# Optimization experiments

Hardware: AMD Instinct MI355X
Metric: run time of the kernel (lower is better)

## Reference

```python
import jax, jax.numpy as jnp
import numpy as np

NB_HEADS = 12


def setup_inputs() -> dict:
    key = jax.random.key(0)
    ks = jax.random.split(key, 6)
    B, S, D, H = 4, 1024, 768, NB_HEADS
    x = jax.random.normal(ks[0], (B, S, D), dtype=jnp.float32)
    Wqkv = jax.random.normal(ks[1], (D, 3 * D), dtype=jnp.float32) * 0.02
    bqkv = jnp.zeros((3 * D,), dtype=jnp.float32)
    Wl = jax.random.normal(ks[2], (H, H), dtype=jnp.float32) * 0.3
    bl = jnp.zeros((H,), dtype=jnp.float32)
    Ww = jax.random.normal(ks[3], (H, H), dtype=jnp.float32) * 0.3
    bw = jnp.zeros((H,), dtype=jnp.float32)
    Wproj = jax.random.normal(ks[4], (D, D), dtype=jnp.float32) * 0.02
    bproj = jnp.zeros((D,), dtype=jnp.float32)
    return {"x": x, "Wqkv": Wqkv, "bqkv": bqkv, "Wl": Wl, "bl": bl,
            "Ww": Ww, "bw": bw, "Wproj": Wproj, "bproj": bproj}


def reference(x, Wqkv, bqkv, Wl, bl, Ww, bw, Wproj, bproj):
    B, S, D = x.shape
    H = NB_HEADS
    dh = D // H
    scale = dh ** (-0.5)
    # qkv projection: [B,S,3D] -> [3,B,H,S,dh]
    qkv = (x @ Wqkv + bqkv).reshape(B, S, 3, H, dh).transpose(2, 0, 3, 1, 4)
    q, k, v = qkv[0] * scale, qkv[1], qkv[2]
    # raw attention logits [B,H,S,S]
    attn = jnp.einsum('bhqd,bhkd->bhqk', q, k)
    # pre-softmax talking-heads mix across head dim (Dense over heads)
    attn = jnp.einsum('bhqk,hg->bgqk', attn, Wl) + bl[None, :, None, None]
    attn = jax.nn.softmax(attn, axis=-1)
    # post-softmax talking-heads mix
    attn = jnp.einsum('bhqk,hg->bgqk', attn, Ww) + bw[None, :, None, None]
    # attention-weighted values -> [B,S,D]
    out = jnp.einsum('bhqk,bhkd->bqhd', attn, v).reshape(B, S, D)
    return out @ Wproj + bproj
```

## Files before the change

kernel.cpp:

```cpp
#include <hip/hip_runtime.h>
#include <cstdint>

#define BB 4
#define SS 1024
#define DD 768
#define HH 12
#define DH 64

typedef unsigned short u16;
typedef unsigned int   u32;
typedef __attribute__((ext_vector_type(8))) short bf16x8;
typedef __attribute__((ext_vector_type(4))) float f32x4;

__device__ __forceinline__ u16 f2bf(float f) {
    u32 u = __float_as_uint(f);
    u += 0x7fffu + ((u >> 16) & 1u);
    return (u16)(u >> 16);
}
__device__ __forceinline__ float b2f(u32 lo16) {
    return __uint_as_float(lo16 << 16);
}
__device__ __forceinline__ u32 pack2(float a, float b) {
    return (u32)f2bf(a) | ((u32)f2bf(b) << 16);
}

#define ASYNC16(gp, lp) __builtin_amdgcn_global_load_lds( \
    (const __attribute__((address_space(1))) void*)(gp),  \
    (__attribute__((address_space(3))) void*)(lp), 16, 0, 0)

template<int BM_, int BN_, class Epi>
__device__ __forceinline__ void mfma_gemm(
    const u16* __restrict__ A, const u16* __restrict__ B,
    int K, int lda, int ldb, int m0, int n0, const Epi& epi)
{
    constexpr int MI = BM_ / 32;
    constexpr int NJ = BN_ / 32;
    __shared__ u16 Alds[BM_ * 32];
    __shared__ u16 Blds[BN_ * 32];

    const int tid  = threadIdx.x;
    const int wave = tid >> 6;
    const int lane = tid & 63;
    const int wr = wave >> 1, wc = wave & 1;

    const int ar = lane >> 2;
    const int ac = (lane & 3) * 8;

    f32x4 acc[MI][NJ] = {};

    for (int k0 = 0; k0 < K; k0 += 32) {
        __syncthreads();
#pragma unroll
        for (int j = 0; j < BM_ / 64; ++j) {
            const int rb = wave * (BM_ / 4) + j * 16;
            ASYNC16(A + (size_t)(m0 + rb + ar) * lda + k0 + ac, &Alds[rb * 32]);
        }
#pragma unroll
        for (int j = 0; j < BN_ / 64; ++j) {
            const int rb = wave * (BN_ / 4) + j * 16;
            ASYNC16(B + (size_t)(n0 + rb + ar) * ldb + k0 + ac, &Blds[rb * 32]);
        }
        __syncthreads();

        bf16x8 af[MI], bfr[NJ];
#pragma unroll
        for (int mi = 0; mi < MI; ++mi)
            af[mi] = *(const bf16x8*)&Alds[(wr * (BM_ / 2) + mi * 16 + (lane & 15)) * 32 + (lane >> 4) * 8];
#pragma unroll
        for (int nj = 0; nj < NJ; ++nj)
            bfr[nj] = *(const bf16x8*)&Blds[(wc * (BN_ / 2) + nj * 16 + (lane & 15)) * 32 + (lane >> 4) * 8];
#pragma unroll
        for (int mi = 0; mi < MI; ++mi)
#pragma unroll
            for (int nj = 0; nj < NJ; ++nj)
                acc[mi][nj] = __builtin_amdgcn_mfma_f32_16x16x32_bf16(
                    af[mi], bfr[nj], acc[mi][nj], 0, 0, 0);
    }

#pragma unroll
    for (int mi = 0; mi < MI; ++mi)
#pragma unroll
        for (int nj = 0; nj < NJ; ++nj)
#pragma unroll
            for (int r = 0; r < 4; ++r)
                epi(m0 + wr * (BM_ / 2) + mi * 16 + (lane >> 4) * 4 + r,
                    n0 + wc * (BN_ / 2) + nj * 16 + (lane & 15),
                    acc[mi][nj][r]);
}

#define CPAD 136

__global__ __launch_bounds__(256) void qkv_gemm_kernel(
    const u16* __restrict__ xb, const u16* __restrict__ Wt,
    const float* __restrict__ bias,
    u16* __restrict__ qb, u16* __restrict__ kb, u16* __restrict__ vb)
{
    __shared__ u16 Alds[128 * 32];
    __shared__ u16 Blds[128 * 32];
    __shared__ u16 Clds[128 * CPAD];

    const int tid  = threadIdx.x;
    const int wave = tid >> 6;
    const int lane = tid & 63;
    const int wr = wave >> 1, wc = wave & 1;
    const int ar = lane >> 2;
    const int ac = (lane & 3) * 8;
    const int m0 = blockIdx.y * 128, n0 = blockIdx.x * 128;

    f32x4 acc[4][4] = {};

    for (int k0 = 0; k0 < DD; k0 += 32) {
        __syncthreads();
#pragma unroll
        for (int j = 0; j < 2; ++j) {
            const int rb = wave * 32 + j * 16;
            ASYNC16(xb + (size_t)(m0 + rb + ar) * DD + k0 + ac, &Alds[rb * 32]);
            ASYNC16(Wt + (size_t)(n0 + rb + ar) * DD + k0 + ac, &Blds[rb * 32]);
        }
        __syncthreads();

        bf16x8 af[4], bfr[4];
#pragma unroll
        for (int mi = 0; mi < 4; ++mi)
            af[mi] = *(const bf16x8*)&Alds[(wr * 64 + mi * 16 + (lane & 15)) * 32 + (lane >> 4) * 8];
#pragma unroll
        for (int nj = 0; nj < 4; ++nj)
            bfr[nj] = *(const bf16x8*)&Blds[(wc * 64 + nj * 16 + (lane & 15)) * 32 + (lane >> 4) * 8];
#pragma unroll
        for (int mi = 0; mi < 4; ++mi)
#pragma unroll
            for (int nj = 0; nj < 4; ++nj)
                acc[mi][nj] = __builtin_amdgcn_mfma_f32_16x16x32_bf16(
                    af[mi], bfr[nj], acc[mi][nj], 0, 0, 0);
    }

    const int c  = n0 / DD;
    const int w0 = n0 - c * DD;
    const int hA = w0 >> 6;
    const float qs = (c == 0) ? 0.125f : 1.0f;
#pragma unroll
    for (int mi = 0; mi < 4; ++mi)
#pragma unroll
        for (int nj = 0; nj < 4; ++nj)
#pragma unroll
            for (int r = 0; r < 4; ++r) {
                const int row = wr * 64 + mi * 16 + (lane >> 4) * 4 + r;
                const int col = wc * 64 + nj * 16 + (lane & 15);
                Clds[row * CPAD + col] = f2bf((acc[mi][nj][r] + bias[n0 + col]) * qs);
            }
    __syncthreads();

    u16* const dst = (c == 0) ? qb : (c == 1) ? kb : vb;
    const int b = m0 >> 10;
#pragma unroll
    for (int j = 0; j < 8; ++j) {
        const int idx = j * 256 + tid;
        const int row = idx >> 4, u4 = idx & 15;
        const int half = u4 >> 3, d8 = u4 & 7;
        const int h = hA + half;
        const int s = (m0 + row) & 1023;
        const uint4 v = *(const uint4*)&Clds[row * CPAD + half * 64 + d8 * 8];
        *(uint4*)&dst[(((size_t)(b * HH + h) << 10) + s) * DH + d8 * 8] = v;
    }
}

__global__ __launch_bounds__(256) void vtrans_kernel(
    const u16* __restrict__ vb, u16* __restrict__ vt)
{
    __shared__ u16 t[64 * 72];
    const int tid = threadIdx.x;
    const int bh = blockIdx.y;
    const int s0 = blockIdx.x * 64;
    const u16* src = vb + ((size_t)bh << 16) + (size_t)s0 * DH;

#pragma unroll
    for (int j = 0; j < 2; ++j) {
        const int idx = j * 256 + tid;
        const int row = idx >> 3, u4 = idx & 7;
        *(uint4*)&t[row * 72 + u4 * 8] = *(const uint4*)&src[row * DH + u4 * 8];
    }
    __syncthreads();

#pragma unroll
    for (int j = 0; j < 2; ++j) {
        const int idx = j * 256 + tid;
        const int d = idx >> 3, u4 = idx & 7;
        u16 tmp[8];
#pragma unroll
        for (int i = 0; i < 8; ++i) tmp[i] = t[(u4 * 8 + i) * 72 + d];
        *(uint4*)&vt[((size_t)bh * DH + d) * SS + s0 + u4 * 8] = *(const uint4*)tmp;
    }
}

__global__ __launch_bounds__(256) void qk_gemm_kernel(
    const u16* __restrict__ qb, const u16* __restrict__ kb,
    u16* __restrict__ attn, int bh0)
{
    __shared__ u16 Alds[128 * 32];
    __shared__ u16 Blds[128 * 32];
    __shared__ u16 Clds[128 * CPAD];

    const int tid  = threadIdx.x;
    const int wave = tid >> 6;
    const int lane = tid & 63;
    const int wr = wave >> 1, wc = wave & 1;
    const int ar = lane >> 2;
    const int ac = (lane & 3) * 8;
    const int m0 = blockIdx.y * 128, n0 = blockIdx.x * 128;

    const int bhL = blockIdx.z;
    const u16* A = qb + (size_t)(bh0 + bhL) * SS * DH;
    const u16* B = kb + (size_t)(bh0 + bhL) * SS * DH;
    u16* C = attn + (size_t)bhL * SS * SS;

    f32x4 acc[4][4] = {};

#pragma unroll
    for (int k0 = 0; k0 < DH; k0 += 32) {
        __syncthreads();
#pragma unroll
        for (int j = 0; j < 2; ++j) {
            const int rb = wave * 32 + j * 16;
            ASYNC16(A + (size_t)(m0 + rb + ar) * DH + k0 + ac, &Alds[rb * 32]);
            ASYNC16(B + (size_t)(n0 + rb + ar) * DH + k0 + ac, &Blds[rb * 32]);
        }
        __syncthreads();

        bf16x8 af[4], bfr[4];
#pragma unroll
        for (int mi = 0; mi < 4; ++mi)
            af[mi] = *(const bf16x8*)&Alds[(wr * 64 + mi * 16 + (lane & 15)) * 32 + (lane >> 4) * 8];
#pragma unroll
        for (int nj = 0; nj < 4; ++nj)
            bfr[nj] = *(const bf16x8*)&Blds[(wc * 64 + nj * 16 + (lane & 15)) * 32 + (lane >> 4) * 8];
#pragma unroll
        for (int mi = 0; mi < 4; ++mi)
#pragma unroll
            for (int nj = 0; nj < 4; ++nj)
                acc[mi][nj] = __builtin_amdgcn_mfma_f32_16x16x32_bf16(
                    af[mi], bfr[nj], acc[mi][nj], 0, 0, 0);
    }

#pragma unroll
    for (int mi = 0; mi < 4; ++mi)
#pragma unroll
        for (int nj = 0; nj < 4; ++nj)
#pragma unroll
            for (int r = 0; r < 4; ++r) {
                const int row = wr * 64 + mi * 16 + (lane >> 4) * 4 + r;
                const int col = wc * 64 + nj * 16 + (lane & 15);
                Clds[row * CPAD + col] = f2bf(acc[mi][nj][r]);
            }
    __syncthreads();

#pragma unroll
    for (int j = 0; j < 8; ++j) {
        const int idx = j * 256 + tid;
        const int row = idx >> 4, u4 = idx & 15;
        *(uint4*)&C[(size_t)(m0 + row) * SS + n0 + u4 * 8] =
            *(const uint4*)&Clds[row * CPAD + u4 * 8];
    }
}


__global__ __launch_bounds__(256) void pv_gemm_kernel(
    const u16* __restrict__ attn2, const u16* __restrict__ vt,
    u16* __restrict__ ctx, int bh0)
{
    const int bhL = blockIdx.z;
    const int bh = bh0 + bhL;
    const int b = bh / HH, h = bh % HH;
    const u16* A = attn2 + (size_t)bhL * SS * SS;
    const u16* B = vt + (size_t)bh * DH * SS;
    u16* C = ctx + (size_t)b * SS * DD + h * DH;
    struct Epi {
        u16* C;
        __device__ void operator()(int m, int n, float v) const {
            C[(size_t)m * DD + n] = f2bf(v);
        }
    } epi{C};
    mfma_gemm<128, 64>(A, B, SS, SS, SS, blockIdx.y * 128, 0, epi);
}

__global__ __launch_bounds__(256) void proj_gemm_kernel(
    const u16* __restrict__ ctx, const u16* __restrict__ Wt,
    const float* __restrict__ bias, float* __restrict__ out)
{
    struct Epi {
        float* out; const float* bias;
        __device__ void operator()(int m, int n, float v) const {
            out[(size_t)m * DD + n] = v + bias[n];
        }
    } epi{out, bias};
    mfma_gemm<128, 64>(ctx, Wt, DD, DD, DD, blockIdx.y * 128, blockIdx.x * 64, epi);
}

__global__ __launch_bounds__(256) void mix_softmax_kernel(
    const u16* __restrict__ attn, u16* __restrict__ attn2,
    const float* __restrict__ Wl, const float* __restrict__ bl,
    const float* __restrict__ Ww, const float* __restrict__ bw)
{
    __shared__ float buf[HH][SS];
    __shared__ float invden[HH];

    const int tid  = threadIdx.x;
    const int wave = tid >> 6;
    const int lane = tid & 63;
    const int bL = blockIdx.x >> 10;
    const int qi = blockIdx.x & (SS - 1);
    const size_t gbase = ((size_t)bL * HH * SS + qi) * SS + tid * 4;
    const int kc = tid * 4;

#pragma unroll
    for (int h = 0; h < HH; ++h) {
        const uint2 u = *(const uint2*)&attn[gbase + (size_t)h * SS * SS];
        float4 f;
        f.x = b2f(u.x & 0xffff); f.y = b2f(u.x >> 16);
        f.z = b2f(u.y & 0xffff); f.w = b2f(u.y >> 16);
        *(float4*)&buf[h][kc] = f;
    }

    {
        float4 vin[HH];
#pragma unroll
        for (int h = 0; h < HH; ++h) vin[h] = *(const float4*)&buf[h][kc];
#pragma unroll
        for (int g = 0; g < HH; ++g) {
            float4 s = {bl[g], bl[g], bl[g], bl[g]};
#pragma unroll
            for (int h = 0; h < HH; ++h) {
                const float w = Wl[h * HH + g];
                s.x += vin[h].x * w; s.y += vin[h].y * w;
                s.z += vin[h].z * w; s.w += vin[h].w * w;
            }
            *(float4*)&buf[g][kc] = s;
        }
    }
    __syncthreads();

#pragma unroll
    for (int rep = 0; rep < 3; ++rep) {
        const int g = rep * 4 + wave;
        float4 v[4];
#pragma unroll
        for (int j = 0; j < 4; ++j)
            v[j] = *(const float4*)&buf[g][lane * 4 + j * 256];

        float ps = 0.f;
#pragma unroll
        for (int j = 0; j < 4; ++j) {
            v[j].x = __expf(v[j].x); v[j].y = __expf(v[j].y);
            v[j].z = __expf(v[j].z); v[j].w = __expf(v[j].w);
            ps += (v[j].x + v[j].y) + (v[j].z + v[j].w);
        }
#pragma unroll
        for (int off = 32; off; off >>= 1) ps += __shfl_xor(ps, off);

#pragma unroll
        for (int j = 0; j < 4; ++j)
            *(float4*)&buf[g][lane * 4 + j * 256] = v[j];
        if (lane == 0) invden[g] = 1.0f / ps;
    }
    __syncthreads();

    {
        float4 vin[HH];
#pragma unroll
        for (int h = 0; h < HH; ++h) {
            float4 t = *(const float4*)&buf[h][kc];
            const float inv = invden[h];
            t.x *= inv; t.y *= inv; t.z *= inv; t.w *= inv;
            vin[h] = t;
        }
#pragma unroll
        for (int g = 0; g < HH; ++g) {
            float4 s = {bw[g], bw[g], bw[g], bw[g]};
#pragma unroll
            for (int h = 0; h < HH; ++h) {
                const float w = Ww[h * HH + g];
                s.x += vin[h].x * w; s.y += vin[h].y * w;
                s.z += vin[h].z * w; s.w += vin[h].w * w;
            }
            uint2 p;
            p.x = pack2(s.x, s.y); p.y = pack2(s.z, s.w);
            *(uint2*)&attn2[gbase + (size_t)g * SS * SS] = p;
        }
    }
}


__global__ __launch_bounds__(256) void cvt_bf16_kernel(
    const float* __restrict__ in, u16* __restrict__ out, int n8)
{
    const int i = blockIdx.x * 256 + threadIdx.x;
    if (i >= n8) return;
    const float4 a = ((const float4*)in)[i * 2];
    const float4 b = ((const float4*)in)[i * 2 + 1];
    uint4 p;
    p.x = pack2(a.x, a.y); p.y = pack2(a.z, a.w);
    p.z = pack2(b.x, b.y); p.w = pack2(b.z, b.w);
    ((uint4*)out)[i] = p;
}

__global__ __launch_bounds__(256) void cvt_transpose_kernel(
    const float* __restrict__ in, u16* __restrict__ out, int R, int C)
{
    __shared__ float t[32][33];
    const int c0 = blockIdx.x * 32, r0 = blockIdx.y * 32;
    const int tr = threadIdx.x >> 3;
    const int tc = (threadIdx.x & 7) * 4;
    const float4 v = *(const float4*)&in[(size_t)(r0 + tr) * C + c0 + tc];
    t[tc + 0][tr] = v.x; t[tc + 1][tr] = v.y;
    t[tc + 2][tr] = v.z; t[tc + 3][tr] = v.w;
    __syncthreads();
    uint2 p;
    p.x = pack2(t[tr][tc + 0], t[tr][tc + 1]);
    p.y = pack2(t[tr][tc + 2], t[tr][tc + 3]);
    *(uint2*)&out[(size_t)(c0 + tr) * R + r0 + tc] = p;
}

extern "C" void kernel_launch(void* const* d_in, const int* in_sizes, int n_in,
                              void* d_out, int out_size, void* d_ws, size_t ws_size,
                              hipStream_t stream)
{
    const float* x     = (const float*)d_in[0];
    const float* Wqkv  = (const float*)d_in[1];
    const float* bqkv  = (const float*)d_in[2];
    const float* Wl    = (const float*)d_in[3];
    const float* bl    = (const float*)d_in[4];
    const float* Ww    = (const float*)d_in[5];
    const float* bw    = (const float*)d_in[6];
    const float* Wproj = (const float*)d_in[7];
    const float* bproj = (const float*)d_in[8];
    float* out = (float*)d_out;

    const size_t N_XB  = (size_t)BB * SS * DD;
    const size_t N_QB  = (size_t)BB * HH * SS * DH;
    const size_t N_WT  = (size_t)DD * 3 * DD;
    const size_t N_WP  = (size_t)DD * DD;
    const size_t N_AT1 = (size_t)HH * SS * SS;

    u16* xb  = (u16*)d_ws;
    u16* qb  = xb  + N_XB;
    u16* kb  = qb  + N_QB;
    u16* vb  = kb  + N_QB;
    u16* vt  = vb  + N_QB;
    u16* ctx = vt  + N_QB;
    u16* Wqkv_t = ctx + N_XB;
    u16* Wproj_t = Wqkv_t + N_WT;
    u16* attn = Wproj_t + N_WP;

    const size_t fixed_bytes = (size_t)(N_XB * 2 + N_QB * 4 + N_WT + N_WP) * 2;
    int b_per = BB;
    while (b_per > 1 &&
           fixed_bytes + (size_t)b_per * N_AT1 * 2 * 2 > ws_size)
        b_per >>= 1;
    const int n_iter = BB / b_per;
    u16* attn2 = attn + (size_t)b_per * N_AT1;

    const dim3 blk(256);

    cvt_bf16_kernel<<<dim3((N_XB / 8 + 255) / 256), blk, 0, stream>>>(x, xb, (int)(N_XB / 8));
    cvt_transpose_kernel<<<dim3(3 * DD / 32, DD / 32), blk, 0, stream>>>(Wqkv, Wqkv_t, DD, 3 * DD);
    cvt_transpose_kernel<<<dim3(DD / 32, DD / 32), blk, 0, stream>>>(Wproj, Wproj_t, DD, DD);

    qkv_gemm_kernel<<<dim3(3 * DD / 128, BB * SS / 128), blk, 0, stream>>>(
        xb, Wqkv_t, bqkv, qb, kb, vb);

    vtrans_kernel<<<dim3(SS / 64, BB * HH), blk, 0, stream>>>(vb, vt);

    for (int it = 0; it < n_iter; ++it) {
        const int bh0 = it * b_per * HH;
        qk_gemm_kernel<<<dim3(SS / 128, SS / 128, b_per * HH), blk, 0, stream>>>(
            qb, kb, attn, bh0);
        mix_softmax_kernel<<<dim3(b_per * SS), blk, 0, stream>>>(
            attn, attn2, Wl, bl, Ww, bw);
        pv_gemm_kernel<<<dim3(1, SS / 128, b_per * HH), blk, 0, stream>>>(
            attn2, vt, ctx, bh0);
    }

    proj_gemm_kernel<<<dim3(DD / 64, BB * SS / 128), blk, 0, stream>>>(
        ctx, Wproj_t, bproj, out);
}
```

Measured before the change: 239.5 us.

## Fuse post-softmax head mix and normalization into the PV GEMM kernel

The softmax kernel now writes unnormalized exponentials in place and stores per-row sums, and it no longer applies the post-softmax talking-heads mix. A new PV kernel loads tiles of the exponentials, normalizes them, applies the Ww head mix in LDS, and runs MFMA against V for all 12 heads of a 16-query block. This removes the second full attention tensor write and read and halves attention workspace, which can allow larger batch chunks. In exchange the mix is recomputed per tile inside the GEMM, the tiles are small with limited reuse of V, and V is read directly from global memory.

```diff
diff --git a/kernel.cpp b/kernel.cpp
--- a/kernel.cpp
+++ b/kernel.cpp
@@ -262,47 +262,11 @@
     }
 }
 
-
-__global__ __launch_bounds__(256) void pv_gemm_kernel(
-    const u16* __restrict__ attn2, const u16* __restrict__ vt,
-    u16* __restrict__ ctx, int bh0)
-{
-    const int bhL = blockIdx.z;
-    const int bh = bh0 + bhL;
-    const int b = bh / HH, h = bh % HH;
-    const u16* A = attn2 + (size_t)bhL * SS * SS;
-    const u16* B = vt + (size_t)bh * DH * SS;
-    u16* C = ctx + (size_t)b * SS * DD + h * DH;
-    struct Epi {
-        u16* C;
-        __device__ void operator()(int m, int n, float v) const {
-            C[(size_t)m * DD + n] = f2bf(v);
-        }
-    } epi{C};
-    mfma_gemm<128, 64>(A, B, SS, SS, SS, blockIdx.y * 128, 0, epi);
-}
-
-__global__ __launch_bounds__(256) void proj_gemm_kernel(
-    const u16* __restrict__ ctx, const u16* __restrict__ Wt,
-    const float* __restrict__ bias, float* __restrict__ out)
-{
-    struct Epi {
-        float* out; const float* bias;
-        __device__ void operator()(int m, int n, float v) const {
-            out[(size_t)m * DD + n] = v + bias[n];
-        }
-    } epi{out, bias};
-    mfma_gemm<128, 64>(ctx, Wt, DD, DD, DD, blockIdx.y * 128, blockIdx.x * 64, epi);
-}
-
 __global__ __launch_bounds__(256) void mix_softmax_kernel(
-    const u16* __restrict__ attn, u16* __restrict__ attn2,
-    const float* __restrict__ Wl, const float* __restrict__ bl,
-    const float* __restrict__ Ww, const float* __restrict__ bw)
+    u16* __restrict__ attn, float* __restrict__ lsum,
+    const float* __restrict__ Wl, const float* __restrict__ bl)
 {
     __shared__ float buf[HH][SS];
-    __shared__ float invden[HH];
-
     const int tid  = threadIdx.x;
     const int wave = tid >> 6;
     const int lane = tid & 63;
@@ -359,33 +323,148 @@
 #pragma unroll
         for (int j = 0; j < 4; ++j)
             *(float4*)&buf[g][lane * 4 + j * 256] = v[j];
-        if (lane == 0) invden[g] = 1.0f / ps;
-    }
-    __syncthreads();
-
+        if (lane == 0)
+            lsum[((size_t)(bL * HH + g) << 10) + qi] = ps;
+    }
+    __syncthreads();
+
+#pragma unroll
+    for (int h = 0; h < HH; ++h) {
+        const float4 t = *(const float4*)&buf[h][kc];
+        uint2 p;
+        p.x = pack2(t.x, t.y); p.y = pack2(t.z, t.w);
+        *(uint2*)&attn[gbase + (size_t)h * SS * SS] = p;
+    }
+}
+
+__global__ __launch_bounds__(512) void pv_mix2_kernel(
+    const u16* __restrict__ e, const float* __restrict__ lsum,
+    const u16* __restrict__ vt, u16* __restrict__ ctx,
+    const float* __restrict__ Ww, const float* __restrict__ bw, int b0)
+{
+    __shared__ u16 smem[12288 + 15360];
+    __shared__ float invL[HH][16];
+    u16* const e_lds = smem;
+    u16* const a2    = smem + 12288;
+
+    const int tid  = threadIdx.x;
+    const int wave = tid >> 6;
+    const int lane = tid & 63;
+    const int q0 = blockIdx.x * 16;
+    const int bL = blockIdx.y;
+    const int b  = b0 + bL;
+
+    if (tid < 192) {
+        const int h = tid >> 4, q = tid & 15;
+        invL[h][q] = 1.0f / lsum[((size_t)(bL * HH + h) << 10) + q0 + q];
+    }
+
+    const int p  = wave >> 2;
+    const int nj = wave & 3;
+    f32x4 acc[6] = {};
+
+    const size_t e_base = ((size_t)bL * HH) << 20;
+
+#pragma unroll
+    for (int j = 0; j < 3; ++j) {
+        const int i = wave * 3 + j;
+        const int r = i * 8 + (lane >> 3);
+        const int h = r >> 4, q = r & 15;
+        ASYNC16(e + e_base + (((size_t)h << 10) + q0 + q) * SS + (lane & 7) * 8,
+                &e_lds[i * 512]);
+    }
+    __syncthreads();
+
+    const int mq = tid >> 5;
+    const int mk = (tid & 31) * 2;
+
+    for (int c = 0; c < 16; ++c) {
+        {
+            float v0[HH], v1[HH];
+#pragma unroll
+            for (int h = 0; h < HH; ++h) {
+                const u32 u = *(const u32*)&e_lds[(h * 16 + mq) * 64 + mk];
+                const float inv = invL[h][mq];
+                v0[h] = b2f(u & 0xffff) * inv;
+                v1[h] = b2f(u >> 16) * inv;
+            }
+#pragma unroll
+            for (int g = 0; g < HH; ++g) {
+                float s0 = bw[g], s1 = s0;
+#pragma unroll
+                for (int h = 0; h < HH; ++h) {
+                    const float w = Ww[h * HH + g];
+                    s0 += v0[h] * w; s1 += v1[h] * w;
+                }
+                *(u32*)&a2[(g * 16 + mq) * 80 + mk] = pack2(s0, s1);
+            }
+        }
+        __syncthreads();
+
+        if (c + 1 < 16) {
+            const int k0 = (c + 1) * 64;
+#pragma unroll
+            for (int j = 0; j < 3; ++j) {
+                const int i = wave * 3 + j;
+                const int r = i * 8 + (lane >> 3);
+                const int h = r >> 4, q = r & 15;
+                ASYNC16(e + e_base + (((size_t)h << 10) + q0 + q) * SS + k0 + (lane & 7) * 8,
+                        &e_lds[i * 512]);
+            }
+        }
+
+#pragma unroll
+        for (int ki = 0; ki < 2; ++ki) {
+            bf16x8 af[6], bfr[6];
+#pragma unroll
+            for (int t = 0; t < 6; ++t) {
+                const int g = p + 2 * t;
+                af[t] = *(const bf16x8*)&a2[(g * 16 + (lane & 15)) * 80 + ki * 32 + (lane >> 4) * 8];
+                const int d = nj * 16 + (lane & 15);
+                bfr[t] = *(const bf16x8*)&vt[(((size_t)(b * HH + g) * DH + d) << 10)
+                                             + c * 64 + ki * 32 + (lane >> 4) * 8];
+            }
+#pragma unroll
+            for (int t = 0; t < 6; ++t)
+                acc[t] = __builtin_amdgcn_mfma_f32_16x16x32_bf16(af[t], bfr[t], acc[t], 0, 0, 0);
+        }
+        __syncthreads();
+    }
+
+    u16* const Clds = smem;
+#pragma unroll
+    for (int t = 0; t < 6; ++t) {
+        const int g = p + 2 * t;
+        const int col = g * 64 + nj * 16 + (lane & 15);
+#pragma unroll
+        for (int r = 0; r < 4; ++r) {
+            const int row = (lane >> 4) * 4 + r;
+            Clds[row * 776 + col] = f2bf(acc[t][r]);
+        }
+    }
+    __syncthreads();
     {
-        float4 vin[HH];
-#pragma unroll
-        for (int h = 0; h < HH; ++h) {
-            float4 t = *(const float4*)&buf[h][kc];
-            const float inv = invden[h];
-            t.x *= inv; t.y *= inv; t.z *= inv; t.w *= inv;
-            vin[h] = t;
-        }
-#pragma unroll
-        for (int g = 0; g < HH; ++g) {
-            float4 s = {bw[g], bw[g], bw[g], bw[g]};
-#pragma unroll
-            for (int h = 0; h < HH; ++h) {
-                const float w = Ww[h * HH + g];
-                s.x += vin[h].x * w; s.y += vin[h].y * w;
-                s.z += vin[h].z * w; s.w += vin[h].w * w;
-            }
-            uint2 p;
-            p.x = pack2(s.x, s.y); p.y = pack2(s.z, s.w);
-            *(uint2*)&attn2[gbase + (size_t)g * SS * SS] = p;
-        }
-    }
+        const int row = tid >> 5;
+#pragma unroll
+        for (int j = 0; j < 3; ++j) {
+            const int u4 = j * 32 + (tid & 31);
+            *(uint4*)&ctx[((size_t)(b * SS + q0 + row)) * DD + u4 * 8] =
+                *(const uint4*)&Clds[row * 776 + u4 * 8];
+        }
+    }
+}
+
+__global__ __launch_bounds__(256) void proj_gemm_kernel(
+    const u16* __restrict__ ctx, const u16* __restrict__ Wt,
+    const float* __restrict__ bias, float* __restrict__ out)
+{
+    struct Epi {
+        float* out; const float* bias;
+        __device__ void operator()(int m, int n, float v) const {
+            out[(size_t)m * DD + n] = v + bias[n];
+        }
+    } epi{out, bias};
+    mfma_gemm<128, 64>(ctx, Wt, DD, DD, DD, blockIdx.y * 128, blockIdx.x * 64, epi);
 }
 
 
@@ -439,6 +518,7 @@
     const size_t N_WT  = (size_t)DD * 3 * DD;
     const size_t N_WP  = (size_t)DD * DD;
     const size_t N_AT1 = (size_t)HH * SS * SS;
+    const size_t N_L1  = (size_t)HH * SS;
 
     u16* xb  = (u16*)d_ws;
     u16* qb  = xb  + N_XB;
@@ -453,10 +533,10 @@
     const size_t fixed_bytes = (size_t)(N_XB * 2 + N_QB * 4 + N_WT + N_WP) * 2;
     int b_per = BB;
     while (b_per > 1 &&
-           fixed_bytes + (size_t)b_per * N_AT1 * 2 * 2 > ws_size)
+           fixed_bytes + (size_t)b_per * (N_AT1 * 2 + N_L1 * 4) > ws_size)
         b_per >>= 1;
     const int n_iter = BB / b_per;
-    u16* attn2 = attn + (size_t)b_per * N_AT1;
+    float* lsum = (float*)(attn + (size_t)b_per * N_AT1);
 
     const dim3 blk(256);
 
@@ -466,17 +546,16 @@
 
     qkv_gemm_kernel<<<dim3(3 * DD / 128, BB * SS / 128), blk, 0, stream>>>(
         xb, Wqkv_t, bqkv, qb, kb, vb);
-
     vtrans_kernel<<<dim3(SS / 64, BB * HH), blk, 0, stream>>>(vb, vt);
 
     for (int it = 0; it < n_iter; ++it) {
-        const int bh0 = it * b_per * HH;
+        const int b0 = it * b_per;
         qk_gemm_kernel<<<dim3(SS / 128, SS / 128, b_per * HH), blk, 0, stream>>>(
-            qb, kb, attn, bh0);
+            qb, kb, attn, b0 * HH);
         mix_softmax_kernel<<<dim3(b_per * SS), blk, 0, stream>>>(
-            attn, attn2, Wl, bl, Ww, bw);
-        pv_gemm_kernel<<<dim3(1, SS / 128, b_per * HH), blk, 0, stream>>>(
-            attn2, vt, ctx, bh0);
+            attn, lsum, Wl, bl);
+        pv_mix2_kernel<<<dim3(SS / 16, b_per), dim3(512), 0, stream>>>(
+            attn, lsum, vt, ctx, Ww, bw, b0);
     }
 
     proj_gemm_kernel<<<dim3(DD / 64, BB * SS / 128), blk, 0, stream>>>(
```

Result: slower. 327.7 us (+36.8%).

## Use MFMA for talking-heads mixes in softmax kernel, shrink PV tiles

Applied to the files above, without the earlier changes.

The two 12x12 head-mixing steps in the mix/softmax kernel now run on bf16 MFMA (16x16x32) over an LDS buffer transposed to [k][head] and padded to 16/32 heads. The softmax denominator is folded into the post-softmax mixing weights, so probabilities are never normalised explicitly. This keeps the intermediate in bf16 LDS instead of fp32, reducing LDS use and VALU FMAs. Separately, the PV GEMM uses 64-row tiles to launch more blocks. Costs include extra bf16 rounding of the logits, exponentials and weights, and possible LDS bank conflicts from the scalar transposed stores.

```diff
diff --git a/kernel.cpp b/kernel.cpp
--- a/kernel.cpp
+++ b/kernel.cpp
@@ -261,7 +261,6 @@
             *(const uint4*)&Clds[row * CPAD + u4 * 8];
     }
 }
-
 
 __global__ __launch_bounds__(256) void pv_gemm_kernel(
     const u16* __restrict__ attn2, const u16* __restrict__ vt,
@@ -279,7 +278,7 @@
             C[(size_t)m * DD + n] = f2bf(v);
         }
     } epi{C};
-    mfma_gemm<128, 64>(A, B, SS, SS, SS, blockIdx.y * 128, 0, epi);
+    mfma_gemm<64, 64>(A, B, SS, SS, SS, blockIdx.y * 64, 0, epi);
 }
 
 __global__ __launch_bounds__(256) void proj_gemm_kernel(
@@ -300,90 +299,116 @@
     const float* __restrict__ Wl, const float* __restrict__ bl,
     const float* __restrict__ Ww, const float* __restrict__ bw)
 {
-    __shared__ float buf[HH][SS];
-    __shared__ float invden[HH];
+    __shared__ __attribute__((aligned(16))) u16 St[1024 * 24 + 8];
+    __shared__ __attribute__((aligned(16))) u16 WlT[16 * 32];
+    __shared__ __attribute__((aligned(16))) u16 WwT[16 * 32];
+    __shared__ float blS[16], bwS[16];
+    __shared__ float redS[4][16];
 
     const int tid  = threadIdx.x;
     const int wave = tid >> 6;
     const int lane = tid & 63;
+    const int p    = lane >> 4;
     const int bL = blockIdx.x >> 10;
     const int qi = blockIdx.x & (SS - 1);
     const size_t gbase = ((size_t)bL * HH * SS + qi) * SS + tid * 4;
-    const int kc = tid * 4;
-
-#pragma unroll
-    for (int h = 0; h < HH; ++h) {
-        const uint2 u = *(const uint2*)&attn[gbase + (size_t)h * SS * SS];
-        float4 f;
-        f.x = b2f(u.x & 0xffff); f.y = b2f(u.x >> 16);
-        f.z = b2f(u.y & 0xffff); f.w = b2f(u.y >> 16);
-        *(float4*)&buf[h][kc] = f;
+
+    for (int e = tid; e < 512; e += 256) {
+        const int g = e >> 5, h = e & 31;
+        WlT[e] = (g < HH && h < HH) ? f2bf(Wl[h * HH + g]) : (u16)0;
+    }
+    if (tid < 16) {
+        blS[tid] = (tid < HH) ? bl[tid] : 0.f;
+        bwS[tid] = (tid < HH) ? bw[tid] : 0.f;
     }
 
     {
-        float4 vin[HH];
-#pragma unroll
-        for (int h = 0; h < HH; ++h) vin[h] = *(const float4*)&buf[h][kc];
+        const int k0 = tid * 4;
+#pragma unroll
+        for (int i = 0; i < 4; ++i) {
+            *(uint2*)&St[(k0 + i) * 24 + 12] = make_uint2(0u, 0u);
+            *(uint4*)&St[(k0 + i) * 24 + 16] = make_uint4(0u, 0u, 0u, 0u);
+        }
+        if (tid == 0)
+            *(uint4*)&St[1024 * 24] = make_uint4(0u, 0u, 0u, 0u);
+#pragma unroll
+        for (int h = 0; h < HH; ++h) {
+            const uint2 u = *(const uint2*)&attn[gbase + (size_t)h * SS * SS];
+            St[(k0 + 0) * 24 + h] = (u16)(u.x & 0xffff);
+            St[(k0 + 1) * 24 + h] = (u16)(u.x >> 16);
+            St[(k0 + 2) * 24 + h] = (u16)(u.y & 0xffff);
+            St[(k0 + 3) * 24 + h] = (u16)(u.y >> 16);
+        }
+    }
+    __syncthreads();
+
+    const bf16x8 af1 = *(const bf16x8*)&WlT[(lane & 15) * 32 + p * 8];
+    float blr[4];
+#pragma unroll
+    for (int r = 0; r < 4; ++r) blr[r] = blS[p * 4 + r];
+    float psum[4] = {0.f, 0.f, 0.f, 0.f};
+    const int kbase = wave * 256;
+    const f32x4 zero = {};
+
+#pragma unroll
+    for (int f = 0; f < 16; ++f) {
+        const int k = kbase + f * 16 + (lane & 15);
+        const bf16x8 bfr = *(const bf16x8*)&St[k * 24 + p * 8];
+        const f32x4 d = __builtin_amdgcn_mfma_f32_16x16x32_bf16(af1, bfr, zero, 0, 0, 0);
+        const float e0 = __expf(d[0] + blr[0]), e1 = __expf(d[1] + blr[1]);
+        const float e2 = __expf(d[2] + blr[2]), e3 = __expf(d[3] + blr[3]);
+        psum[0] += e0; psum[1] += e1; psum[2] += e2; psum[3] += e3;
+        uint2 pk;
+        pk.x = pack2(e0, e1); pk.y = pack2(e2, e3);
+        *(uint2*)&St[k * 24 + p * 4] = pk;
+    }
+
+#pragma unroll
+    for (int r = 0; r < 4; ++r)
+#pragma unroll
+        for (int off = 1; off < 16; off <<= 1)
+            psum[r] += __shfl_xor(psum[r], off);
+    if ((lane & 15) == 0)
+#pragma unroll
+        for (int r = 0; r < 4; ++r) redS[wave][p * 4 + r] = psum[r];
+    __syncthreads();
+
+    for (int e = tid; e < 512; e += 256) {
+        const int g = e >> 5, h = e & 31;
+        u16 v = 0;
+        if (g < HH && h < HH) {
+            const float l = (redS[0][h] + redS[1][h]) + (redS[2][h] + redS[3][h]);
+            v = f2bf(Ww[h * HH + g] / l);
+        }
+        WwT[e] = v;
+    }
+    __syncthreads();
+
+    const bf16x8 af2 = *(const bf16x8*)&WwT[(lane & 15) * 32 + p * 8];
+    float bwr[4];
+#pragma unroll
+    for (int r = 0; r < 4; ++r) bwr[r] = bwS[p * 4 + r];
+
+#pragma unroll
+    for (int f = 0; f < 16; ++f) {
+        const int k = kbase + f * 16 + (lane & 15);
+        const bf16x8 bfr = *(const bf16x8*)&St[k * 24 + p * 8];
+        const f32x4 d = __builtin_amdgcn_mfma_f32_16x16x32_bf16(af2, bfr, zero, 0, 0, 0);
+        uint2 pk;
+        pk.x = pack2(d[0] + bwr[0], d[1] + bwr[1]);
+        pk.y = pack2(d[2] + bwr[2], d[3] + bwr[3]);
+        *(uint2*)&St[k * 24 + p * 4] = pk;
+    }
+    __syncthreads();
+
+    {
+        const int k0 = tid * 4;
 #pragma unroll
         for (int g = 0; g < HH; ++g) {
-            float4 s = {bl[g], bl[g], bl[g], bl[g]};
-#pragma unroll
-            for (int h = 0; h < HH; ++h) {
-                const float w = Wl[h * HH + g];
-                s.x += vin[h].x * w; s.y += vin[h].y * w;
-                s.z += vin[h].z * w; s.w += vin[h].w * w;
-            }
-            *(float4*)&buf[g][kc] = s;
-        }
-    }
-    __syncthreads();
-
-#pragma unroll
-    for (int rep = 0; rep < 3; ++rep) {
-        const int g = rep * 4 + wave;
-        float4 v[4];
-#pragma unroll
-        for (int j = 0; j < 4; ++j)
-            v[j] = *(const float4*)&buf[g][lane * 4 + j * 256];
-
-        float ps = 0.f;
-#pragma unroll
-        for (int j = 0; j < 4; ++j) {
-            v[j].x = __expf(v[j].x); v[j].y = __expf(v[j].y);
-            v[j].z = __expf(v[j].z); v[j].w = __expf(v[j].w);
-            ps += (v[j].x + v[j].y) + (v[j].z + v[j].w);
-        }
-#pragma unroll
-        for (int off = 32; off; off >>= 1) ps += __shfl_xor(ps, off);
-
-#pragma unroll
-        for (int j = 0; j < 4; ++j)
-            *(float4*)&buf[g][lane * 4 + j * 256] = v[j];
-        if (lane == 0) invden[g] = 1.0f / ps;
-    }
-    __syncthreads();
-
-    {
-        float4 vin[HH];
-#pragma unroll
-        for (int h = 0; h < HH; ++h) {
-            float4 t = *(const float4*)&buf[h][kc];
-            const float inv = invden[h];
-            t.x *= inv; t.y *= inv; t.z *= inv; t.w *= inv;
-            vin[h] = t;
-        }
-#pragma unroll
-        for (int g = 0; g < HH; ++g) {
-            float4 s = {bw[g], bw[g], bw[g], bw[g]};
-#pragma unroll
-            for (int h = 0; h < HH; ++h) {
-                const float w = Ww[h * HH + g];
-                s.x += vin[h].x * w; s.y += vin[h].y * w;
-                s.z += vin[h].z * w; s.w += vin[h].w * w;
-            }
-            uint2 p;
-            p.x = pack2(s.x, s.y); p.y = pack2(s.z, s.w);
-            *(uint2*)&attn2[gbase + (size_t)g * SS * SS] = p;
+            uint2 o;
+            o.x = (u32)St[(k0 + 0) * 24 + g] | ((u32)St[(k0 + 1) * 24 + g] << 16);
+            o.y = (u32)St[(k0 + 2) * 24 + g] | ((u32)St[(k0 + 3) * 24 + g] << 16);
+            *(uint2*)&attn2[gbase + (size_t)g * SS * SS] = o;
         }
     }
 }
@@ -466,7 +491,6 @@
 
     qkv_gemm_kernel<<<dim3(3 * DD / 128, BB * SS / 128), blk, 0, stream>>>(
         xb, Wqkv_t, bqkv, qb, kb, vb);
-
     vtrans_kernel<<<dim3(SS / 64, BB * HH), blk, 0, stream>>>(vb, vt);
 
     for (int it = 0; it < n_iter; ++it) {
@@ -475,7 +499,7 @@
             qb, kb, attn, bh0);
         mix_softmax_kernel<<<dim3(b_per * SS), blk, 0, stream>>>(
             attn, attn2, Wl, bl, Ww, bw);
-        pv_gemm_kernel<<<dim3(1, SS / 128, b_per * HH), blk, 0, stream>>>(
+        pv_gemm_kernel<<<dim3(1, SS / 64, b_per * HH), blk, 0, stream>>>(
             attn2, vt, ctx, bh0);
     }
 
```

Measured after the change: 243.6 us. About the same (+1.7%).
